# Kernel optimization log

Measured on AMD Instinct MI355X. Metric: run time of the kernel, lower is better.

Reference implementation:

```python
import jax, jax.numpy as jnp
import numpy as np

D, H, DFF = 128, 8, 256
W0, T0, S0 = 7200, 36, 13
W1, T1, S1 = 720, 144, 29


def _level(W, T, stride):
    # deterministic variable-length windows: window w holds nv[w] valid voxels
    nv = 1 + (np.arange(W) * stride) % T            # in [1, T]
    valid = np.arange(T)[None, :] < nv[:, None]      # [W, T]
    inds = np.nonzero(valid.reshape(-1))[0].astype(np.int32)  # flat positions in [0, W*T)
    return jnp.asarray(inds), jnp.asarray(~valid)    # key_padding_mask: True = pad


def setup_inputs() -> dict:
    key = jax.random.key(0)
    ks = jax.random.split(key, 8)
    inds0, mask0 = _level(W0, T0, S0)
    inds1, mask1 = _level(W1, T1, S1)
    N = int(inds0.shape[0] + inds1.shape[0])  # 133200 + 52200 = 185400
    sc = 0.02
    return {
        'src': jax.random.normal(ks[0], (N, D), jnp.float32),
        'pos0': jax.random.normal(ks[1], (W0, T0, D), jnp.float32),
        'pos1': jax.random.normal(ks[2], (W1, T1, D), jnp.float32),
        'inds0': inds0, 'inds1': inds1, 'mask0': mask0, 'mask1': mask1,
        'in_proj_w': sc * jax.random.normal(ks[3], (3 * D, D), jnp.float32),
        'in_proj_b': jnp.zeros((3 * D,), jnp.float32),
        'out_proj_w': sc * jax.random.normal(ks[4], (D, D), jnp.float32),
        'out_proj_b': jnp.zeros((D,), jnp.float32),
        'lin1_w': sc * jax.random.normal(ks[5], (DFF, D), jnp.float32),
        'lin1_b': jnp.zeros((DFF,), jnp.float32),
        'lin2_w': sc * jax.random.normal(ks[6], (D, DFF), jnp.float32),
        'lin2_b': jnp.zeros((D,), jnp.float32),
        'ln1_g': jnp.ones((D,), jnp.float32), 'ln1_b': jnp.zeros((D,), jnp.float32),
        'ln2_g': jnp.ones((D,), jnp.float32), 'ln2_b': jnp.zeros((D,), jnp.float32),
    }


def _ln(x, g, b, eps=1e-5):
    m = x.mean(-1, keepdims=True)
    v = x.var(-1, keepdims=True)
    return (x - m) * jax.lax.rsqrt(v + eps) * g + b


def _mha(feat, pos, mask, Wi, bi, Wo, bo):
    # torch nn.MultiheadAttention math; q = k = feat + pos, v = feat
    Wn, T, _ = feat.shape
    dh = D // H
    Wq, Wk, Wv = jnp.split(Wi, 3, axis=0)
    bq, bk, bv = jnp.split(bi, 3, axis=0)
    qk = feat + pos
    q = (qk @ Wq.T + bq).reshape(Wn, T, H, dh)
    k = (qk @ Wk.T + bk).reshape(Wn, T, H, dh)
    v = (feat @ Wv.T + bv).reshape(Wn, T, H, dh)
    s = jnp.einsum('wqhd,wkhd->whqk', q, k) * (1.0 / np.sqrt(dh))
    s = jnp.where(mask[:, None, None, :], jnp.asarray(-1e9, s.dtype), s)
    a = jax.nn.softmax(s, axis=-1)
    o = jnp.einsum('whqk,wkhd->wqhd', a, v).reshape(Wn, T, D)
    return o @ Wo.T + bo


def reference(src, pos0, pos1, inds0, inds1, mask0, mask1,
              in_proj_w, in_proj_b, out_proj_w, out_proj_b,
              lin1_w, lin1_b, lin2_w, lin2_b,
              ln1_g, ln1_b, ln2_g, ln2_b):
    N0 = inds0.shape[0]
    # flat2window: scatter flat voxel feats into padded per-level window buffers
    f0 = jnp.zeros((W0 * T0, D), src.dtype).at[inds0].set(src[:N0]).reshape(W0, T0, D)
    f1 = jnp.zeros((W1 * T1, D), src.dtype).at[inds1].set(src[N0:]).reshape(W1, T1, D)
    o0 = _mha(f0, pos0, mask0, in_proj_w, in_proj_b, out_proj_w, out_proj_b)
    o1 = _mha(f1, pos1, mask1, in_proj_w, in_proj_b, out_proj_w, out_proj_b)
    # window2flat: gather valid positions back to flat layout
    src2 = jnp.concatenate([o0.reshape(-1, D)[inds0], o1.reshape(-1, D)[inds1]], axis=0)
    x = _ln(src + src2, ln1_g, ln1_b)
    y = jax.nn.relu(x @ lin1_w.T + lin1_b) @ lin2_w.T + lin2_b
    return _ln(x + y, ln2_g, ln2_b)
```

## Files before the change

### kernel.cpp

```cpp
#include <hip/hip_runtime.h>
#include <stdint.h>

typedef uint16_t u16;
typedef short bf16x8 __attribute__((ext_vector_type(8)));
typedef float f32x4 __attribute__((ext_vector_type(4)));

constexpr int kD  = 128;
constexpr int kN  = 185400;
constexpr int kN0 = 133200;

constexpr int  kWoOff  = 49152;
constexpr int  kW1Off  = 65536;
constexpr int  kW2Off  = 98304;
constexpr long kPosOff = 131072;
constexpr long kQkvOff = 501872;

__device__ __forceinline__ float bf2f(u16 x){
  uint32_t u = ((uint32_t)x) << 16; float f; __builtin_memcpy(&f, &u, 4); return f;
}
__device__ __forceinline__ u16 f2bf(float f){
  uint32_t u; __builtin_memcpy(&u, &f, 4);
  u += 0x7fffu + ((u >> 16) & 1u);
  return (u16)(u >> 16);
}
__device__ __forceinline__ bf16x8 ld8(const u16* p){ return *(const bf16x8*)p; }
__device__ __forceinline__ bf16x8 cvt8(const float* p){
  f32x4 a = *(const f32x4*)p, b = *(const f32x4*)(p + 4);
  bf16x8 o;
#pragma unroll
  for (int i = 0; i < 4; i++){ o[i] = (short)f2bf(a[i]); o[4+i] = (short)f2bf(b[i]); }
  return o;
}
__device__ __forceinline__ bf16x8 cvt8sum(const float* x, const float* y){
  f32x4 a = *(const f32x4*)x, b = *(const f32x4*)(x + 4);
  f32x4 c = *(const f32x4*)y, d = *(const f32x4*)(y + 4);
  bf16x8 o;
#pragma unroll
  for (int i = 0; i < 4; i++){ o[i] = (short)f2bf(a[i] + c[i]); o[4+i] = (short)f2bf(b[i] + d[i]); }
  return o;
}
__device__ __forceinline__ f32x4 mfma16(bf16x8 a, bf16x8 b, f32x4 c){
  return __builtin_amdgcn_mfma_f32_16x16x32_bf16(a, b, c, 0, 0, 0);
}

__global__ __launch_bounds__(256) void cvtw_kernel(
    const float* __restrict__ Wi, const float* __restrict__ Wo,
    const float* __restrict__ W1, const float* __restrict__ W2,
    u16* __restrict__ out){
  int base = (blockIdx.x * 256 + threadIdx.x) * 8;
  const float* src; int off;
  if (base < kWoOff){ src = Wi; off = base; }
  else if (base < kW1Off){ src = Wo; off = base - kWoOff; }
  else if (base < kW2Off){ src = W1; off = base - kW1Off; }
  else { src = W2; off = base - kW2Off; }
  *(bf16x8*)(out + base) = cvt8(src + off);
}

__global__ __launch_bounds__(256) void posmap_kernel(int* __restrict__ posidx){
  int b = blockIdx.x;
  if (b < 7200){
    int w = b;
    int r = w % 36;
    int n = 1 + (w * 13) % 36;
    int fr = 0;
    for (int i = 0; i < r; i++) fr += (i * 13) % 36;
    int off = w + (w / 36) * 630 + fr;
    for (int t = threadIdx.x; t < n; t += 256) posidx[off + t] = w * 36 + t;
  } else {
    int w = b - 7200;
    int r = w % 144;
    int n = 1 + (w * 29) % 144;
    int fr = 0;
    for (int i = 0; i < r; i++) fr += (i * 29) % 144;
    int off = kN0 + w + (w / 144) * 10296 + fr;
    for (int t = threadIdx.x; t < n; t += 256) posidx[off + t] = w * 144 + t;
  }
}

__global__ __launch_bounds__(256) __attribute__((amdgpu_waves_per_eu(2, 4)))
void qkv_kernel(const float* __restrict__ src,
                const float* __restrict__ pos0, const float* __restrict__ pos1,
                const int* __restrict__ posidx,
                const u16* __restrict__ Wib, const float* __restrict__ bi,
                u16* __restrict__ qkv){
  __shared__ __align__(16) u16 st[4][16*384];
  int wave = threadIdx.x >> 6, lane = threadIdx.x & 63;
  int m16 = lane & 15, quad = lane >> 4;
  long tb = (long)blockIdx.x * 4 + wave;
  long rb = tb * 16;
  if (rb < kN){
    long ar = rb + m16; if (ar >= kN) ar = kN - 1;
    const float* sp = src + ar * kD + quad * 8;
    int pidx = posidx[ar];
    const float* pbase = (ar < kN0) ? pos0 : pos1;
    const float* pp = pbase + (long)pidx * kD + quad * 8;
    bf16x8 aqk[4], av[4];
#pragma unroll
    for (int ks = 0; ks < 4; ks++){ av[ks] = cvt8(sp + ks*32); aqk[ks] = cvt8sum(sp + ks*32, pp + ks*32); }
    u16* tile = st[wave];
#pragma unroll
    for (int ct = 0; ct < 8; ct++){
      int colc = ct * 16 + m16;
      const u16* wq = Wib + (long)colc * kD + quad * 8;
      f32x4 aq = {0,0,0,0}, ak = {0,0,0,0}, avv = {0,0,0,0};
#pragma unroll
      for (int ks = 0; ks < 4; ks++){
        aq  = mfma16(aqk[ks], ld8(wq + ks*32),         aq);
        ak  = mfma16(aqk[ks], ld8(wq + 16384 + ks*32), ak);
        avv = mfma16(av[ks],  ld8(wq + 32768 + ks*32), avv);
      }
      float cbq = bi[colc], cbk = bi[128+colc], cbv = bi[256+colc];
#pragma unroll
      for (int rr = 0; rr < 4; rr++){
        int trow = quad * 4 + rr;
        tile[trow*384 + colc]       = f2bf(aq[rr]  + cbq);
        tile[trow*384 + 128 + colc] = f2bf(ak[rr]  + cbk);
        tile[trow*384 + 256 + colc] = f2bf(avv[rr] + cbv);
      }
    }
    int nrows = (int)min((long)16, kN - rb);
    int elems = nrows * 384;
    u16* gp = qkv + rb * 384;
    for (int e = lane * 8; e < elems; e += 512)
      *(bf16x8*)(gp + e) = ld8(tile + e);
  }
}

__global__ __launch_bounds__(256) __attribute__((amdgpu_waves_per_eu(4, 8)))
void attn0_kernel(const u16* __restrict__ qkv, float* __restrict__ O){
  __shared__ __align__(16) u16 ksm[36*128], vsm[36*128];
  int w = blockIdx.x;
  int r = w % 36;
  int n = 1 + (w * 13) % 36;
  int fr = 0;
  for (int i = 0; i < r; i++) fr += (i * 13) % 36;
  int off = w + (w / 36) * 630 + fr;

  int nel = n * 128;
  for (int e = threadIdx.x * 8; e < nel; e += 2048){
    int row = e >> 7, col = e & 127;
    const u16* rp = qkv + (long)(off + row) * 384;
    *(bf16x8*)(ksm + e) = ld8(rp + 128 + col);
    *(bf16x8*)(vsm + e) = ld8(rp + 256 + col);
  }
  __syncthreads();
  int total = n * 8;
  for (int idx = threadIdx.x; idx < total; idx += 256){
    int qi = idx >> 3, h = idx & 7;
    const u16* qp = qkv + (long)(off + qi) * 384 + h * 16;
    bf16x8 q0 = ld8(qp), q1 = ld8(qp + 8);
    float qv[16];
#pragma unroll
    for (int i = 0; i < 8; i++){ qv[i] = 0.25f*bf2f((u16)q0[i]); qv[8+i] = 0.25f*bf2f((u16)q1[i]); }
    const u16* kbp = ksm + h*16;
    const u16* vbp = vsm + h*16;
    float l = 0.f, acc[16];
#pragma unroll
    for (int i = 0; i < 16; i++) acc[i] = 0.f;
    bf16x8 ck0 = ld8(kbp), ck1 = ld8(kbp+8), cv0 = ld8(vbp), cv1 = ld8(vbp+8);
    for (int j = 0; j < n; j++){
      bf16x8 k0 = ck0, k1 = ck1, v0 = cv0, v1 = cv1;
      int jn = min(j+1, n-1);
      ck0 = ld8(kbp + jn*kD); ck1 = ld8(kbp + jn*kD + 8);
      cv0 = ld8(vbp + jn*kD); cv1 = ld8(vbp + jn*kD + 8);
      float s0=0.f, s1=0.f, s2=0.f, s3=0.f;
#pragma unroll
      for (int i = 0; i < 4; i++){
        s0 += qv[i]   *bf2f((u16)k0[i]);
        s1 += qv[4+i] *bf2f((u16)k0[4+i]);
        s2 += qv[8+i] *bf2f((u16)k1[i]);
        s3 += qv[12+i]*bf2f((u16)k1[4+i]);
      }
      float p = __expf(fminf((s0+s1)+(s2+s3), 30.f));
      l += p;
#pragma unroll
      for (int i = 0; i < 8; i++){
        acc[i]   += p*bf2f((u16)v0[i]);
        acc[8+i] += p*bf2f((u16)v1[i]);
      }
    }
    float rl = 1.f / l;
    float* op = O + (long)(off + qi)*kD + h*16;
    f32x4 o0, o1, o2, o3;
#pragma unroll
    for (int i = 0; i < 4; i++){
      o0[i] = acc[i]*rl; o1[i] = acc[4+i]*rl; o2[i] = acc[8+i]*rl; o3[i] = acc[12+i]*rl;
    }
    *(f32x4*)op = o0; *(f32x4*)(op+4) = o1; *(f32x4*)(op+8) = o2; *(f32x4*)(op+12) = o3;
  }
}

__global__ __launch_bounds__(256) __attribute__((amdgpu_waves_per_eu(4, 8)))
void attn1_kernel(const u16* __restrict__ qkv, float* __restrict__ O){
  __shared__ __align__(16) u16 ksm[64*128], vsm[64*128];
  int w = blockIdx.x / 5;
  int qc = blockIdx.x % 5;
  int n = 1 + (w * 29) % 144;
  if (qc * 32 >= n) return;
  int r = w % 144;
  int fr = 0;
  for (int i = 0; i < r; i++) fr += (i * 29) % 144;
  int off = kN0 + w + (w / 144) * 10296 + fr;

  int h = threadIdx.x & 7;
  int ql = threadIdx.x >> 3;
  int qi = qc * 32 + ql;
  bool active = qi < n;
  int qrow = off + (active ? qi : n - 1);
  const u16* qp = qkv + (long)qrow * 384 + h * 16;
  bf16x8 q0 = ld8(qp), q1 = ld8(qp + 8);
  float qv[16];
#pragma unroll
  for (int i = 0; i < 8; i++){ qv[i] = 0.25f*bf2f((u16)q0[i]); qv[8+i] = 0.25f*bf2f((u16)q1[i]); }
  float l = 0.f, acc[16];
#pragma unroll
  for (int i = 0; i < 16; i++) acc[i] = 0.f;

  int nchunks = (n + 63) / 64;
  for (int c = 0; c < nchunks; c++){
    int cnt = min(64, n - c * 64);
    __syncthreads();
    int base = off + c * 64;
    int nel = cnt * 128;
    for (int e = threadIdx.x * 8; e < nel; e += 2048){
      int row = e >> 7, col = e & 127;
      const u16* rp = qkv + (long)(base + row) * 384;
      *(bf16x8*)(ksm + e) = ld8(rp + 128 + col);
      *(bf16x8*)(vsm + e) = ld8(rp + 256 + col);
    }
    __syncthreads();
    const u16* kbp = ksm + h*16;
    const u16* vbp = vsm + h*16;
    bf16x8 ck0 = ld8(kbp), ck1 = ld8(kbp+8), cv0 = ld8(vbp), cv1 = ld8(vbp+8);
    for (int j = 0; j < cnt; j++){
      bf16x8 k0 = ck0, k1 = ck1, v0 = cv0, v1 = cv1;
      int jn = min(j+1, cnt-1);
      ck0 = ld8(kbp + jn*kD); ck1 = ld8(kbp + jn*kD + 8);
      cv0 = ld8(vbp + jn*kD); cv1 = ld8(vbp + jn*kD + 8);
      float s0=0.f, s1=0.f, s2=0.f, s3=0.f;
#pragma unroll
      for (int i = 0; i < 4; i++){
        s0 += qv[i]   *bf2f((u16)k0[i]);
        s1 += qv[4+i] *bf2f((u16)k0[4+i]);
        s2 += qv[8+i] *bf2f((u16)k1[i]);
        s3 += qv[12+i]*bf2f((u16)k1[4+i]);
      }
      float p = __expf(fminf((s0+s1)+(s2+s3), 30.f));
      l += p;
#pragma unroll
      for (int i = 0; i < 8; i++){
        acc[i]   += p*bf2f((u16)v0[i]);
        acc[8+i] += p*bf2f((u16)v1[i]);
      }
    }
  }
  if (active){
    float rl = 1.f / l;
    float* op = O + (long)(off + qi)*kD + h*16;
    f32x4 o0, o1, o2, o3;
#pragma unroll
    for (int i = 0; i < 4; i++){
      o0[i] = acc[i]*rl; o1[i] = acc[4+i]*rl; o2[i] = acc[8+i]*rl; o3[i] = acc[12+i]*rl;
    }
    *(f32x4*)op = o0; *(f32x4*)(op+4) = o1; *(f32x4*)(op+8) = o2; *(f32x4*)(op+12) = o3;
  }
}

__global__ __launch_bounds__(256, 3) void outproj_ln_kernel(
    const float* __restrict__ src, const u16* __restrict__ Wob,
    const float* __restrict__ bo, const float* __restrict__ g,
    const float* __restrict__ be, float* __restrict__ OX){
  int lane = threadIdx.x & 63, wave = threadIdx.x >> 6;
  int m16 = lane & 15, quad = lane >> 4;
  int rowbase = blockIdx.x * 64 + wave * 16;
  int arow = rowbase + m16; if (arow >= kN) arow = kN - 1;
  const float* Ap = OX + (long)arow * kD + quad * 8;
  bf16x8 af[4];
#pragma unroll
  for (int ks = 0; ks < 4; ks++) af[ks] = cvt8(Ap + ks*32);
  float vals[8][4];
#pragma unroll
  for (int ct = 0; ct < 8; ct++){
    int colc = ct * 16 + m16;
    const u16* wp = Wob + (long)colc * kD + quad * 8;
    f32x4 acc = {0,0,0,0};
#pragma unroll
    for (int ks = 0; ks < 4; ks++) acc = mfma16(af[ks], ld8(wp + ks*32), acc);
    float bb = bo[colc];
#pragma unroll
    for (int rr = 0; rr < 4; rr++){
      int row = rowbase + quad*4 + rr; if (row >= kN) row = kN - 1;
      vals[ct][rr] = acc[rr] + bb + src[(long)row * kD + colc];
    }
  }
  float mean[4], rstd[4];
#pragma unroll
  for (int rr = 0; rr < 4; rr++){
    float s = 0.f, q2 = 0.f;
#pragma unroll
    for (int ct = 0; ct < 8; ct++){ s += vals[ct][rr]; q2 += vals[ct][rr]*vals[ct][rr]; }
#pragma unroll
    for (int msk = 1; msk < 16; msk <<= 1){ s += __shfl_xor(s, msk, 64); q2 += __shfl_xor(q2, msk, 64); }
    mean[rr] = s * (1.f/128.f);
    float var = q2 * (1.f/128.f) - mean[rr]*mean[rr];
    rstd[rr] = rsqrtf(var + 1e-5f);
  }
#pragma unroll
  for (int ct = 0; ct < 8; ct++){
    int colc = ct * 16 + m16;
    float gg = g[colc], bb = be[colc];
#pragma unroll
    for (int rr = 0; rr < 4; rr++){
      int row = rowbase + quad*4 + rr;
      if (row < kN)
        OX[(long)row * kD + colc] = (vals[ct][rr] - mean[rr]) * rstd[rr] * gg + bb;
    }
  }
}

__global__ __launch_bounds__(256, 3) void ffn_kernel(
    const u16* __restrict__ W1b, const float* __restrict__ b1,
    const u16* __restrict__ W2b, const float* __restrict__ b2,
    const float* __restrict__ g, const float* __restrict__ be,
    float* __restrict__ XO){
  __shared__ __align__(16) u16 xs[64*128];
  __shared__ __align__(16) u16 hs[64*264];
  int rb = blockIdx.x * 64;
  for (int c = threadIdx.x; c < 1024; c += 256){
    int row = c >> 4, col = (c & 15) * 8;
    int grow = rb + row; if (grow >= kN) grow = kN - 1;
    *(bf16x8*)(xs + row*kD + col) = cvt8(XO + (long)grow * kD + col);
  }
  __syncthreads();
  int lane = threadIdx.x & 63, wave = threadIdx.x >> 6;
  int m16 = lane & 15, quad = lane >> 4;
  int lrow = wave * 16 + m16;
  bf16x8 af[4];
#pragma unroll
  for (int ks = 0; ks < 4; ks++) af[ks] = ld8(xs + lrow*kD + quad*8 + ks*32);
#pragma unroll
  for (int ct2 = 0; ct2 < 16; ct2++){
    int col2 = ct2 * 16 + m16;
    const u16* wp = W1b + (long)col2 * kD + quad * 8;
    f32x4 acc = {0,0,0,0};
#pragma unroll
    for (int ks = 0; ks < 4; ks++) acc = mfma16(af[ks], ld8(wp + ks*32), acc);
    float bb = b1[col2];
#pragma unroll
    for (int rr = 0; rr < 4; rr++)
      hs[(wave*16 + quad*4 + rr)*264 + col2] = f2bf(fmaxf(acc[rr] + bb, 0.f));
  }
  __syncthreads();
  bf16x8 hf[8];
#pragma unroll
  for (int ks2 = 0; ks2 < 8; ks2++) hf[ks2] = ld8(hs + lrow*264 + quad*8 + ks2*32);
  float vals[8][4];
#pragma unroll
  for (int ct = 0; ct < 8; ct++){
    int colc = ct * 16 + m16;
    const u16* wp = W2b + (long)colc * 256 + quad * 8;
    f32x4 acc = {0,0,0,0};
#pragma unroll
    for (int ks2 = 0; ks2 < 8; ks2++) acc = mfma16(hf[ks2], ld8(wp + ks2*32), acc);
    float bb = b2[colc];
#pragma unroll
    for (int rr = 0; rr < 4; rr++)
      vals[ct][rr] = acc[rr] + bb + bf2f(xs[(wave*16 + quad*4 + rr)*kD + colc]);
  }
  float mean[4], rstd[4];
#pragma unroll
  for (int rr = 0; rr < 4; rr++){
    float s = 0.f, q2 = 0.f;
#pragma unroll
    for (int ct = 0; ct < 8; ct++){ s += vals[ct][rr]; q2 += vals[ct][rr]*vals[ct][rr]; }
#pragma unroll
    for (int msk = 1; msk < 16; msk <<= 1){ s += __shfl_xor(s, msk, 64); q2 += __shfl_xor(q2, msk, 64); }
    mean[rr] = s * (1.f/128.f);
    float var = q2 * (1.f/128.f) - mean[rr]*mean[rr];
    rstd[rr] = rsqrtf(var + 1e-5f);
  }
#pragma unroll
  for (int ct = 0; ct < 8; ct++){
    int colc = ct * 16 + m16;
    float gg = g[colc], bb = be[colc];
#pragma unroll
    for (int rr = 0; rr < 4; rr++){
      int row = rb + wave*16 + quad*4 + rr;
      if (row < kN)
        XO[(long)row * kD + colc] = (vals[ct][rr] - mean[rr]) * rstd[rr] * gg + bb;
    }
  }
}

extern "C" void kernel_launch(void* const* d_in, const int* in_sizes, int n_in,
                              void* d_out, int out_size, void* d_ws, size_t ws_size,
                              hipStream_t stream){
  const float* src  = (const float*)d_in[0];
  const float* pos0 = (const float*)d_in[1];
  const float* pos1 = (const float*)d_in[2];
  const float* Wi  = (const float*)d_in[7];
  const float* bi  = (const float*)d_in[8];
  const float* Wo  = (const float*)d_in[9];
  const float* bo  = (const float*)d_in[10];
  const float* W1  = (const float*)d_in[11];
  const float* b1  = (const float*)d_in[12];
  const float* W2  = (const float*)d_in[13];
  const float* b2  = (const float*)d_in[14];
  const float* g1  = (const float*)d_in[15];
  const float* be1 = (const float*)d_in[16];
  const float* g2  = (const float*)d_in[17];
  const float* be2 = (const float*)d_in[18];
  float* out = (float*)d_out;
  u16* wsb = (u16*)d_ws;
  int* pmap = (int*)(wsb + kPosOff);
  u16* qkvw = wsb + kQkvOff;

  dim3 blk(256);
  cvtw_kernel<<<dim3(64), blk, 0, stream>>>(Wi, Wo, W1, W2, wsb);
  posmap_kernel<<<dim3(7920), blk, 0, stream>>>(pmap);
  qkv_kernel<<<dim3(2897), blk, 0, stream>>>(src, pos0, pos1, pmap, wsb, bi, qkvw);
  attn0_kernel<<<dim3(7200), blk, 0, stream>>>(qkvw, out);
  attn1_kernel<<<dim3(3600), blk, 0, stream>>>(qkvw, out);
  outproj_ln_kernel<<<dim3(2897), blk, 0, stream>>>(src, wsb + kWoOff, bo, g1, be1, out);
  ffn_kernel<<<dim3(2897), blk, 0, stream>>>(wsb + kW1Off, b1, wsb + kW2Off, b2, g2, be2, out);
}
```

Baseline: 894.4 us.

## Fuse out-projection LayerNorm and FFN into one kernel

Merges the out-projection+residual+LayerNorm kernel with the FFN+LayerNorm kernel so the normalized activations stay in shared memory as bf16 instead of being written to and re-read from global memory in fp32. Removes the block-level barriers since each wave only touches its own rows, and adjusts shared-memory row padding. Changes occupancy hints, which with higher register pressure may reduce concurrency.

```diff
diff --git a/kernel.cpp b/kernel.cpp
--- a/kernel.cpp
+++ b/kernel.cpp
@@ -266,15 +266,24 @@
   }
 }
 
-__global__ __launch_bounds__(256, 3) void outproj_ln_kernel(
+__global__ __launch_bounds__(256) __attribute__((amdgpu_waves_per_eu(2, 4)))
+void oln_ffn_kernel(
     const float* __restrict__ src, const u16* __restrict__ Wob,
-    const float* __restrict__ bo, const float* __restrict__ g,
-    const float* __restrict__ be, float* __restrict__ OX){
+    const float* __restrict__ bo, const float* __restrict__ g1,
+    const float* __restrict__ be1,
+    const u16* __restrict__ W1b, const float* __restrict__ b1,
+    const u16* __restrict__ W2b, const float* __restrict__ b2,
+    const float* __restrict__ g2, const float* __restrict__ be2,
+    float* __restrict__ OX){
+  __shared__ __align__(16) u16 xs[64*132];
+  __shared__ __align__(16) u16 hs[64*260];
   int lane = threadIdx.x & 63, wave = threadIdx.x >> 6;
   int m16 = lane & 15, quad = lane >> 4;
   int rowbase = blockIdx.x * 64 + wave * 16;
-  int arow = rowbase + m16; if (arow >= kN) arow = kN - 1;
-  const float* Ap = OX + (long)arow * kD + quad * 8;
+  int lrow = wave * 16 + m16;
+
+  long arow = rowbase + m16; if (arow >= kN) arow = kN - 1;
+  const float* Ap = OX + arow * kD + quad * 8;
   bf16x8 af[4];
 #pragma unroll
   for (int ks = 0; ks < 4; ks++) af[ks] = cvt8(Ap + ks*32);
@@ -289,8 +298,8 @@
     float bb = bo[colc];
 #pragma unroll
     for (int rr = 0; rr < 4; rr++){
-      int row = rowbase + quad*4 + rr; if (row >= kN) row = kN - 1;
-      vals[ct][rr] = acc[rr] + bb + src[(long)row * kD + colc];
+      long row = rowbase + quad*4 + rr; if (row >= kN) row = kN - 1;
+      vals[ct][rr] = acc[rr] + bb + src[row * kD + colc];
     }
   }
   float mean[4], rstd[4];
@@ -308,53 +317,31 @@
 #pragma unroll
   for (int ct = 0; ct < 8; ct++){
     int colc = ct * 16 + m16;
-    float gg = g[colc], bb = be[colc];
-#pragma unroll
-    for (int rr = 0; rr < 4; rr++){
-      int row = rowbase + quad*4 + rr;
-      if (row < kN)
-        OX[(long)row * kD + colc] = (vals[ct][rr] - mean[rr]) * rstd[rr] * gg + bb;
-    }
-  }
-}
-
-__global__ __launch_bounds__(256, 3) void ffn_kernel(
-    const u16* __restrict__ W1b, const float* __restrict__ b1,
-    const u16* __restrict__ W2b, const float* __restrict__ b2,
-    const float* __restrict__ g, const float* __restrict__ be,
-    float* __restrict__ XO){
-  __shared__ __align__(16) u16 xs[64*128];
-  __shared__ __align__(16) u16 hs[64*264];
-  int rb = blockIdx.x * 64;
-  for (int c = threadIdx.x; c < 1024; c += 256){
-    int row = c >> 4, col = (c & 15) * 8;
-    int grow = rb + row; if (grow >= kN) grow = kN - 1;
-    *(bf16x8*)(xs + row*kD + col) = cvt8(XO + (long)grow * kD + col);
-  }
-  __syncthreads();
-  int lane = threadIdx.x & 63, wave = threadIdx.x >> 6;
-  int m16 = lane & 15, quad = lane >> 4;
-  int lrow = wave * 16 + m16;
-  bf16x8 af[4];
-#pragma unroll
-  for (int ks = 0; ks < 4; ks++) af[ks] = ld8(xs + lrow*kD + quad*8 + ks*32);
+    float gg = g1[colc], bb = be1[colc];
+#pragma unroll
+    for (int rr = 0; rr < 4; rr++)
+      xs[(wave*16 + quad*4 + rr)*132 + colc] = f2bf((vals[ct][rr] - mean[rr]) * rstd[rr] * gg + bb);
+  }
+
+  bf16x8 xf[4];
+#pragma unroll
+  for (int ks = 0; ks < 4; ks++) xf[ks] = ld8(xs + lrow*132 + quad*8 + ks*32);
 #pragma unroll
   for (int ct2 = 0; ct2 < 16; ct2++){
     int col2 = ct2 * 16 + m16;
     const u16* wp = W1b + (long)col2 * kD + quad * 8;
     f32x4 acc = {0,0,0,0};
 #pragma unroll
-    for (int ks = 0; ks < 4; ks++) acc = mfma16(af[ks], ld8(wp + ks*32), acc);
+    for (int ks = 0; ks < 4; ks++) acc = mfma16(xf[ks], ld8(wp + ks*32), acc);
     float bb = b1[col2];
 #pragma unroll
     for (int rr = 0; rr < 4; rr++)
-      hs[(wave*16 + quad*4 + rr)*264 + col2] = f2bf(fmaxf(acc[rr] + bb, 0.f));
-  }
-  __syncthreads();
+      hs[(wave*16 + quad*4 + rr)*260 + col2] = f2bf(fmaxf(acc[rr] + bb, 0.f));
+  }
+
   bf16x8 hf[8];
 #pragma unroll
-  for (int ks2 = 0; ks2 < 8; ks2++) hf[ks2] = ld8(hs + lrow*264 + quad*8 + ks2*32);
-  float vals[8][4];
+  for (int ks2 = 0; ks2 < 8; ks2++) hf[ks2] = ld8(hs + lrow*260 + quad*8 + ks2*32);
 #pragma unroll
   for (int ct = 0; ct < 8; ct++){
     int colc = ct * 16 + m16;
@@ -365,9 +352,8 @@
     float bb = b2[colc];
 #pragma unroll
     for (int rr = 0; rr < 4; rr++)
-      vals[ct][rr] = acc[rr] + bb + bf2f(xs[(wave*16 + quad*4 + rr)*kD + colc]);
-  }
-  float mean[4], rstd[4];
+      vals[ct][rr] = acc[rr] + bb + bf2f(xs[(wave*16 + quad*4 + rr)*132 + colc]);
+  }
 #pragma unroll
   for (int rr = 0; rr < 4; rr++){
     float s = 0.f, q2 = 0.f;
@@ -382,12 +368,12 @@
 #pragma unroll
   for (int ct = 0; ct < 8; ct++){
     int colc = ct * 16 + m16;
-    float gg = g[colc], bb = be[colc];
+    float gg = g2[colc], bb = be2[colc];
 #pragma unroll
     for (int rr = 0; rr < 4; rr++){
-      int row = rb + wave*16 + quad*4 + rr;
+      long row = rowbase + quad*4 + rr;
       if (row < kN)
-        XO[(long)row * kD + colc] = (vals[ct][rr] - mean[rr]) * rstd[rr] * gg + bb;
+        OX[row * kD + colc] = (vals[ct][rr] - mean[rr]) * rstd[rr] * gg + bb;
     }
   }
 }
@@ -421,6 +407,7 @@
   qkv_kernel<<<dim3(2897), blk, 0, stream>>>(src, pos0, pos1, pmap, wsb, bi, qkvw);
   attn0_kernel<<<dim3(7200), blk, 0, stream>>>(qkvw, out);
   attn1_kernel<<<dim3(3600), blk, 0, stream>>>(qkvw, out);
-  outproj_ln_kernel<<<dim3(2897), blk, 0, stream>>>(src, wsb + kWoOff, bo, g1, be1, out);
-  ffn_kernel<<<dim3(2897), blk, 0, stream>>>(wsb + kW1Off, b1, wsb + kW2Off, b2, g2, be2, out);
-}
+  oln_ffn_kernel<<<dim3(2897), blk, 0, stream>>>(src, wsb + kWoOff, bo, g1, be1,
+                                                 wsb + kW1Off, b1, wsb + kW2Off, b2,
+                                                 g2, be2, out);
+}
```

New measurement: 864.3 us. 1.03x faster.
